# Performance work log

Hardware: AMD Instinct MI355X
Metric: run time of the kernel (lower is better)

Reference implementation:

```python
import jax, jax.numpy as jnp
import numpy as np

NPOINT = 2048
RADIUS = 0.4
NSAMPLE = 32
BN_EPS = 1e-5


def setup_inputs() -> dict:
    key = jax.random.key(0)
    ks = jax.random.split(key, 6)
    B, N, C = 8, 8192, 64
    xyz = jax.random.normal(ks[0], (B, N, 3), jnp.float32)
    points = jax.random.normal(ks[1], (B, N, C), jnp.float32)
    W1 = jax.random.normal(ks[2], (3 + C, 64), jnp.float32) * 0.1
    W2 = jax.random.normal(ks[3], (64, 64), jnp.float32) * 0.1
    W3 = jax.random.normal(ks[4], (64, 128), jnp.float32) * 0.1
    return dict(
        xyz=xyz, points=points,
        W1=W1, g1=jnp.ones(64), b1=jnp.zeros(64),
        W2=W2, g2=jnp.ones(64), b2=jnp.zeros(64),
        W3=W3, g3=jnp.ones(128), b3=jnp.zeros(128),
    )


def _furthest_point_sample(xyz, npoint):
    # xyz: (B, N, 3) -> (B, npoint) int32. Sequential max-min scan, batched.
    B, N, _ = xyz.shape

    def step(carry, _):
        dists, last = carry
        p = jnp.take_along_axis(xyz, last[:, None, None], axis=1)  # (B,1,3)
        d2 = jnp.sum((xyz - p) ** 2, axis=-1)                       # (B,N)
        dists = jnp.minimum(dists, d2)
        nxt = jnp.argmax(dists, axis=-1).astype(jnp.int32)
        return (dists, nxt), nxt

    init = (jnp.full((B, N), 1e10, xyz.dtype), jnp.zeros((B,), jnp.int32))
    _, idx = jax.lax.scan(step, init, None, length=npoint - 1)      # (npoint-1, B)
    idx = jnp.concatenate([jnp.zeros((1, B), jnp.int32), idx], axis=0)
    return idx.T                                                    # (B, npoint)


def _ball_query(xyz, new_xyz, radius, nsample):
    # For each centroid take the first nsample point indices (in original order)
    # within `radius`; pad with the first found index (CUDA ball_query semantics).
    B, N, _ = xyz.shape
    d2 = jnp.sum((new_xyz[:, :, None, :] - xyz[:, None, :, :]) ** 2, axis=-1)  # (B,S,N)
    mask = d2 < radius * radius
    key = jnp.where(mask, jnp.arange(N, dtype=jnp.int32), N)
    srt = jnp.sort(key, axis=-1)[..., :nsample]                     # (B,S,K)
    first = srt[..., :1]
    first = jnp.where(first == N, 0, first)                         # empty ball -> index 0
    return jnp.where(srt == N, first, srt)


def _gather(pts, idx):
    # pts: (B,N,D), idx: (B,...) -> (B,...,D)
    return jax.vmap(lambda p, i: p[i])(pts, idx)


def reference(xyz, points, W1, g1, b1, W2, g2, b2, W3, g3, b3):
    fps_idx = _furthest_point_sample(xyz, NPOINT)                   # (B,S)
    new_xyz = _gather(xyz, fps_idx)                                 # (B,S,3)
    idx = _ball_query(xyz, new_xyz, RADIUS, NSAMPLE)                # (B,S,K)
    grouped_xyz = _gather(xyz, idx) - new_xyz[:, :, None, :]        # (B,S,K,3)
    grouped_pts = _gather(points, idx)                              # (B,S,K,C)
    feats = jnp.concatenate([grouped_xyz, grouped_pts], axis=-1)    # (B,S,K,3+C)
    for W, g, b in ((W1, g1, b1), (W2, g2, b2), (W3, g3, b3)):
        feats = feats @ W                                           # 1x1 conv
        m = feats.mean(axis=(0, 1, 2))
        v = feats.var(axis=(0, 1, 2))                               # biased, torch BN train mode
        feats = g * (feats - m) * jax.lax.rsqrt(v + BN_EPS) + b
        feats = jax.nn.relu(feats)
    new_points = feats.max(axis=2)                                  # max over nsample -> (B,S,mlp[-1])
    return new_xyz, new_points
```

## Files before the change

### kernel.cpp

```cpp
#include <hip/hip_runtime.h>

constexpr int B_ = 8, N_ = 8192, NPOINT_ = 2048, NSAMPLE_ = 32;
constexpr int M_ROWS = B_ * NPOINT_ * NSAMPLE_;
constexpr int NGROUP = B_ * NPOINT_;
constexpr size_t OFF_NXF   = 0;
constexpr size_t OFF_IDX   = 196608;
constexpr size_t OFF_WF    = 1245184;
constexpr size_t OFF_GB    = 1311488;
constexpr size_t OFF_STATS = 1313536;
constexpr size_t OFF_NP    = 1315584;
constexpr size_t OFF_FLAG  = 1317632;
constexpr size_t OFF_MAXB  = 2097152;

__device__ __forceinline__ float bf2f(unsigned short u) {
  union { unsigned u; float f; } x; x.u = ((unsigned)u) << 16; return x.f;
}
__device__ __forceinline__ float lo16f(unsigned u) {
  union { unsigned u; float f; } x; x.u = u << 16; return x.f;
}
__device__ __forceinline__ float hi16f(unsigned u) {
  union { unsigned u; float f; } x; x.u = u & 0xffff0000u; return x.f;
}
__device__ __forceinline__ unsigned short f2bf(float f) {
  union { float f; unsigned u; } x; x.f = f;
  unsigned u = x.u + 0x7FFFu + ((x.u >> 16) & 1u);
  return (unsigned short)(u >> 16);
}
__device__ __forceinline__ int f2i(float f) {
  union { float f; int i; } x; x.f = f; return x.i;
}
__device__ __forceinline__ float i2f(int i) {
  union { int i; float f; } x; x.i = i; return x.f;
}
__device__ __forceinline__ void unpack8(uint4 u, float* x) {
  x[0] = bf2f((unsigned short)(u.x & 0xffffu)); x[1] = bf2f((unsigned short)(u.x >> 16));
  x[2] = bf2f((unsigned short)(u.y & 0xffffu)); x[3] = bf2f((unsigned short)(u.y >> 16));
  x[4] = bf2f((unsigned short)(u.z & 0xffffu)); x[5] = bf2f((unsigned short)(u.z >> 16));
  x[6] = bf2f((unsigned short)(u.w & 0xffffu)); x[7] = bf2f((unsigned short)(u.w >> 16));
}
__device__ __forceinline__ float ldf(const void* p, size_t i, bool bf) {
  return bf ? bf2f(((const unsigned short*)p)[i]) : ((const float*)p)[i];
}
__device__ __forceinline__ void stf(void* p, size_t i, bool bf, float v) {
  if (bf) ((unsigned short*)p)[i] = f2bf(v);
  else    ((float*)p)[i] = v;
}

template <int CTRL>
__device__ __forceinline__ float dpp_maxf(float v) {
  int n = __builtin_amdgcn_update_dpp(0, f2i(v), CTRL, 0xF, 0xF, true);
  return fmaxf(v, i2f(n));
}

extern "C" __global__ void detect_kernel(const unsigned short* __restrict__ xyz,
                                         int* __restrict__ flag) {
  if (threadIdx.x == 0 && blockIdx.x == 0) {
    int sane = 0;
    for (int k = 0; k < 32; ++k) {
      int e = (xyz[2 * k] >> 7) & 0xff;
      if (e >= 90 && e <= 140) ++sane;
    }
    *flag = (sane >= 24) ? 1 : 0;
  }
}

extern "C" __global__ void prep_kernel(
    const void* W1, const void* W2, const void* W3,
    const void* g1, const void* b1, const void* g2, const void* b2,
    const void* g3, const void* b3,
    float* __restrict__ wf, float* __restrict__ gb, const int* __restrict__ flag) {
  const bool bf = (*flag != 0);
  int i = blockIdx.x * 256 + threadIdx.x;
  if (i < 4288)       wf[i] = ldf(W1, i, bf);
  else if (i < 8384)  wf[i] = ldf(W2, i - 4288, bf);
  else if (i < 16576) wf[i] = ldf(W3, i - 8384, bf);
  else if (i < 17088) {
    int k = i - 16576; float v;
    if (k < 64)       v = ldf(g1, k, bf);
    else if (k < 128) v = ldf(b1, k - 64, bf);
    else if (k < 192) v = ldf(g2, k - 128, bf);
    else if (k < 256) v = ldf(b2, k - 192, bf);
    else if (k < 384) v = ldf(g3, k - 256, bf);
    else              v = ldf(b3, k - 384, bf);
    gb[k] = v;
  }
}

extern "C" __global__ void conv_kernel(const void* xyz, float* __restrict__ sxyz,
                                       const int* __restrict__ flag) {
  const bool bf = (*flag != 0);
  int i = blockIdx.x * 256 + threadIdx.x;
  if (i < B_ * N_) {
    sxyz[i]             = ldf(xyz, (size_t)i * 3 + 0, bf);
    sxyz[B_*N_ + i]     = ldf(xyz, (size_t)i * 3 + 1, bf);
    sxyz[2*B_*N_ + i]   = ldf(xyz, (size_t)i * 3 + 2, bf);
  }
}

template <bool BF>
__device__ __forceinline__ void fps_body(
    const void* xyz, void* out, float* __restrict__ nxf, float4* slots) {
#pragma clang fp contract(off)
  const int b = blockIdx.x;
  const int t = threadIdx.x;
  const int lane = t & 63, w = t >> 6;
  const size_t base = (size_t)b * N_ * 3;
  float px[8], py[8], pz[8], d[8];
  if (BF) {
    const uint4* xp = (const uint4*)((const unsigned short*)xyz + base) + t * 3;
    unsigned cc[12];
#pragma unroll
    for (int m = 0; m < 3; ++m) {
      uint4 u = xp[m];
      cc[4*m+0] = u.x; cc[4*m+1] = u.y; cc[4*m+2] = u.z; cc[4*m+3] = u.w;
    }
#pragma unroll
    for (int k = 0; k < 8; ++k) {
      if ((k & 1) == 0) {
        unsigned ra = cc[(3*k) >> 1], rb = cc[((3*k) >> 1) + 1];
        px[k] = lo16f(ra); py[k] = hi16f(ra); pz[k] = lo16f(rb);
      } else {
        unsigned ra = cc[(3*k - 1) >> 1], rb = cc[(3*k + 1) >> 1];
        px[k] = hi16f(ra); py[k] = lo16f(rb); pz[k] = hi16f(rb);
      }
    }
  } else {
#pragma unroll
    for (int k = 0; k < 8; ++k) {
      int i = t * 8 + k;
      px[k] = ((const float*)xyz)[base + i*3 + 0];
      py[k] = ((const float*)xyz)[base + i*3 + 1];
      pz[k] = ((const float*)xyz)[base + i*3 + 2];
    }
  }
#pragma unroll
  for (int k = 0; k < 8; ++k) d[k] = 1e10f;
  float s0x=0.f,s0y=0.f,s0z=0.f, s1x=0.f,s1y=0.f,s1z=0.f;
  float p0, p1, p2;
  if (BF) {
    const unsigned short* xp16 = (const unsigned short*)xyz + base;
    p0 = bf2f(xp16[0]); p1 = bf2f(xp16[1]); p2 = bf2f(xp16[2]);
  } else {
    p0 = ((const float*)xyz)[base + 0];
    p1 = ((const float*)xyz)[base + 1];
    p2 = ((const float*)xyz)[base + 2];
  }
  if (t == 0) { s0x = p0; s0y = p1; s0z = p2; }
  for (int j = 1; j < NPOINT_; ++j) {
    float bv = -1.0f;
#pragma unroll
    for (int k = 0; k < 8; ++k) {
      float dx = px[k] - p0, dy = py[k] - p1, dz = pz[k] - p2;
      float d2 = (dx*dx + dy*dy) + dz*dz;
      float dn = fminf(d[k], d2);
      d[k] = dn;
      bv = fmaxf(bv, dn);
    }
    float g = bv;
    g = dpp_maxf<0xB1>(g);
    g = dpp_maxf<0x4E>(g);
    g = dpp_maxf<0x141>(g);
    g = dpp_maxf<0x140>(g);
    g = dpp_maxf<0x142>(g);
    g = dpp_maxf<0x143>(g);
    float wmax = i2f(__builtin_amdgcn_readlane(f2i(g), 63));
    unsigned long long hm = __ballot(bv == wmax);
    int sl = (int)__builtin_ctzll(hm);
    const int pb = (j & 1) << 4;
    if (lane == sl) {
      int bk = 0;
#pragma unroll
      for (int k = 7; k >= 1; --k)
        if (d[k] == bv) bk = k;
      float cx = px[0], cy = py[0], cz = pz[0];
#pragma unroll
      for (int k = 1; k < 8; ++k)
        if (bk == k) { cx = px[k]; cy = py[k]; cz = pz[k]; }
      slots[pb + w] = make_float4(bv, cx, cy, cz);
    }
    __syncthreads();
    float4 kc = slots[pb + (lane & 15)];
    float m2 = kc.x;
    m2 = dpp_maxf<0xB1>(m2);
    m2 = dpp_maxf<0x4E>(m2);
    m2 = dpp_maxf<0x141>(m2);
    m2 = dpp_maxf<0x140>(m2);
    unsigned long long bm = __ballot(kc.x == m2);
    int s2 = (int)__builtin_ctzll(bm);
    p0 = i2f(__builtin_amdgcn_readlane(f2i(kc.y), s2));
    p1 = i2f(__builtin_amdgcn_readlane(f2i(kc.z), s2));
    p2 = i2f(__builtin_amdgcn_readlane(f2i(kc.w), s2));
    if (t == (j & 1023)) {
      if ((j >> 10) == 0) { s0x = p0; s0y = p1; s0z = p2; }
      else                { s1x = p0; s1y = p1; s1z = p2; }
    }
  }
  const bool bfrt = BF;
#pragma unroll
  for (int s = 0; s < 2; ++s) {
    float cx = (s==0)?s0x:s1x;
    float cy = (s==0)?s0y:s1y;
    float cz = (s==0)?s0z:s1z;
    size_t o = ((size_t)b * NPOINT_ + s * 1024 + t) * 3;
    nxf[o+0] = cx; nxf[o+1] = cy; nxf[o+2] = cz;
    stf(out, o+0, bfrt, cx); stf(out, o+1, bfrt, cy); stf(out, o+2, bfrt, cz);
  }
}

extern "C" __global__ void __launch_bounds__(1024, 4) fps_kernel(
    const void* xyz, void* out, float* __restrict__ nxf,
    const int* __restrict__ flag) {
  __shared__ float4 slots[32];
  if (*flag != 0) fps_body<true>(xyz, out, nxf, slots);
  else            fps_body<false>(xyz, out, nxf, slots);
}

extern "C" __global__ void __launch_bounds__(256) ballq_kernel(
    const float* __restrict__ sxyz, const float* __restrict__ nxf,
    unsigned short* __restrict__ idxout) {
#pragma clang fp contract(off)
  const int gw = (int)((blockIdx.x * 256 + threadIdx.x) >> 6);
  const int lane = threadIdx.x & 63;
  const int b = gw >> 11;
  const int j = gw & (NPOINT_ - 1);
  const float* sx = sxyz;
  const float* sy = sxyz + B_ * N_;
  const float* sz = sxyz + 2 * B_ * N_;
  const size_t pbase = (size_t)b * N_;
  const size_t co = ((size_t)b * NPOINT_ + j) * 3;
  const float c0 = nxf[co], c1 = nxf[co+1], c2 = nxf[co+2];
  unsigned short* out = idxout + (size_t)gw * NSAMPLE_;
  int cnt = 0, first = -1;
  for (int c = 0; c < N_/64 && cnt < NSAMPLE_; ++c) {
    int i = c * 64 + lane;
    float dx = sx[pbase + i] - c0;
    float dy = sy[pbase + i] - c1;
    float dz = sz[pbase + i] - c2;
    float d2 = (dx*dx + dy*dy) + dz*dz;
    bool hit = d2 < 0.16f;
    unsigned long long m = __ballot(hit);
    if (m) {
      if (first < 0) first = c * 64 + (int)__builtin_ctzll(m);
      int rank = __builtin_amdgcn_mbcnt_hi(
          (unsigned)(m >> 32), __builtin_amdgcn_mbcnt_lo((unsigned)m, 0));
      if (hit) {
        int pos = cnt + rank;
        if (pos < NSAMPLE_) out[pos] = (unsigned short)i;
      }
      cnt += __builtin_popcountll(m);
    }
  }
  if (first < 0) first = 0;
  if (lane < NSAMPLE_ && lane >= cnt) out[lane] = (unsigned short)first;
}

__device__ __forceinline__ void l1_row(
    const void* xyz, const void* points, const float* __restrict__ nxf,
    const unsigned short* __restrict__ idx, const float* __restrict__ wf,
    int r, bool bf, float* acc) {
  const int b = r >> 16;
  const int j = (r >> 5) & (NPOINT_ - 1);
  const int i = idx[r];
  const size_t pt = (size_t)b * N_ + i;
  const float* cp = nxf + ((size_t)b * NPOINT_ + j) * 3;
  float f0 = ldf(xyz, pt*3 + 0, bf) - cp[0];
  float f1 = ldf(xyz, pt*3 + 1, bf) - cp[1];
  float f2 = ldf(xyz, pt*3 + 2, bf) - cp[2];
#pragma unroll
  for (int c = 0; c < 64; ++c)
    acc[c] = fmaf(f0, wf[c], fmaf(f1, wf[64+c], f2 * wf[128+c]));
  const float* wp = wf + 192;
  if (bf) {
    const uint4* pp = (const uint4*)((const unsigned short*)points + pt * 64);
#pragma unroll
    for (int s = 0; s < 8; ++s) {
      uint4 u = pp[s];
      float x[8]; unpack8(u, x);
#pragma unroll
      for (int kk = 0; kk < 8; ++kk)
#pragma unroll
        for (int c = 0; c < 64; ++c)
          acc[c] = fmaf(x[kk], wp[(s*8+kk)*64 + c], acc[c]);
    }
  } else {
    const float4* pp = (const float4*)((const float*)points + pt * 64);
#pragma unroll
    for (int s = 0; s < 16; ++s) {
      float4 u = pp[s];
      float x[4] = {u.x, u.y, u.z, u.w};
#pragma unroll
      for (int kk = 0; kk < 4; ++kk)
#pragma unroll
        for (int c = 0; c < 64; ++c)
          acc[c] = fmaf(x[kk], wp[(s*4+kk)*64 + c], acc[c]);
    }
  }
}

template <int LDW>
__device__ __forceinline__ void mm64(const float* v, const float* __restrict__ w,
                                     float* acc) {
#pragma unroll
  for (int ch = 0; ch < 64; ++ch)
#pragma unroll
    for (int c = 0; c < 64; ++c)
      acc[c] = fmaf(v[ch], w[ch*LDW + c], acc[c]);
}

__device__ __forceinline__ void bnrelu64(float* v, const float* __restrict__ np0) {
#pragma unroll
  for (int c = 0; c < 64; ++c)
    v[c] = fmaxf(fmaf(v[c], np0[c], np0[64 + c]), 0.f);
}

__device__ __forceinline__ void commit_stats64(float* a, float* __restrict__ stats) {
  float q[64];
#pragma unroll
  for (int c = 0; c < 64; ++c) q[c] = a[c] * a[c];
#pragma unroll
  for (int off = 1; off < 64; off <<= 1)
#pragma unroll
    for (int c = 0; c < 64; ++c) {
      a[c] += __shfl_xor(a[c], off);
      q[c] += __shfl_xor(q[c], off);
    }
  __shared__ float LS[4][64], LQ[4][64];
  const int t = threadIdx.x, w = t >> 6;
  if ((t & 63) == 0) {
#pragma unroll
    for (int c = 0; c < 64; ++c) { LS[w][c] = a[c]; LQ[w][c] = q[c]; }
  }
  __syncthreads();
  if (t < 64) {
    atomicAdd(&stats[t],      LS[0][t] + LS[1][t] + LS[2][t] + LS[3][t]);
    atomicAdd(&stats[64 + t], LQ[0][t] + LQ[1][t] + LQ[2][t] + LQ[3][t]);
  }
}

extern "C" __global__ void __launch_bounds__(256) p1_kernel(
    const void* xyz, const void* points, const float* __restrict__ nxf,
    const unsigned short* __restrict__ idx, const float* __restrict__ wf,
    float* __restrict__ stats, const int* __restrict__ flag) {
  const bool bf = (*flag != 0);
  const int r = blockIdx.x * 256 + threadIdx.x;
  float acc[64];
  l1_row(xyz, points, nxf, idx, wf, r, bf, acc);
  commit_stats64(acc, stats);
}

extern "C" __global__ void __launch_bounds__(256, 2) p2_kernel(
    const void* xyz, const void* points, const float* __restrict__ nxf,
    const unsigned short* __restrict__ idx, const float* __restrict__ wf,
    const float* __restrict__ w2, const float* __restrict__ np1,
    float* __restrict__ stats, const int* __restrict__ flag) {
  const bool bf = (*flag != 0);
  const int r = blockIdx.x * 256 + threadIdx.x;
  float v[64];
  l1_row(xyz, points, nxf, idx, wf, r, bf, v);
  bnrelu64(v, np1);
  float acc[64];
#pragma unroll
  for (int c = 0; c < 64; ++c) acc[c] = 0.f;
  mm64<64>(v, w2, acc);
  commit_stats64(acc, stats);
}

extern "C" __global__ void __launch_bounds__(256, 2) p3_kernel(
    const void* xyz, const void* points, const float* __restrict__ nxf,
    const unsigned short* __restrict__ idx, const float* __restrict__ wf,
    const float* __restrict__ w2, const float* __restrict__ w3,
    const float* __restrict__ np1, const float* __restrict__ np2,
    unsigned short* __restrict__ maxb, float* __restrict__ stats,
    const int* __restrict__ flag) {
  const bool bf = (*flag != 0);
  const int t = threadIdx.x, lane = t & 63, w = t >> 6;
  const int h = __builtin_amdgcn_readfirstlane(w & 1);
  const int g = blockIdx.x * 4 + (w >> 1) * 2 + (lane >> 5);
  const int r = g * 32 + (lane & 31);
  float v[64];
  l1_row(xyz, points, nxf, idx, wf, r, bf, v);
  bnrelu64(v, np1);
  float y2[64];
#pragma unroll
  for (int c = 0; c < 64; ++c) y2[c] = 0.f;
  mm64<64>(v, w2, y2);
  bnrelu64(y2, np2);
  const float* w3h = w3 + h * 64;
  float y3[64];
#pragma unroll
  for (int c = 0; c < 64; ++c) y3[c] = 0.f;
  mm64<128>(y2, w3h, y3);
  float* s = v; float* q = y2;
#pragma unroll
  for (int c = 0; c < 64; ++c) { s[c] = y3[c]; q[c] = y3[c] * y3[c]; }
#pragma unroll
  for (int off = 1; off <= 16; off <<= 1)
#pragma unroll
    for (int c = 0; c < 64; ++c)
      y3[c] = fmaxf(y3[c], __shfl_xor(y3[c], off));
  if ((lane & 31) == 0) {
    unsigned short* mo = maxb + (size_t)g * 128 + h * 64;
#pragma unroll
    for (int c = 0; c < 64; ++c) mo[c] = f2bf(y3[c]);
  }
#pragma unroll
  for (int off = 1; off < 64; off <<= 1)
#pragma unroll
    for (int c = 0; c < 64; ++c) {
      s[c] += __shfl_xor(s[c], off);
      q[c] += __shfl_xor(q[c], off);
    }
  __shared__ float LS[4][64], LQ[4][64];
  if (lane == 0) {
#pragma unroll
    for (int c = 0; c < 64; ++c) { LS[w][c] = s[c]; LQ[w][c] = q[c]; }
  }
  __syncthreads();
  if (t < 128) {
    int hh = t >> 6, cl = t & 63;
    atomicAdd(&stats[t],       LS[hh][cl] + LS[hh+2][cl]);
    atomicAdd(&stats[128 + t], LQ[hh][cl] + LQ[hh+2][cl]);
  }
}

extern "C" __global__ void nparam_kernel(
    const float* __restrict__ stats, const float* __restrict__ g,
    const float* __restrict__ bb, float* __restrict__ npar, int Cc) {
  int c = threadIdx.x;
  if (c < Cc) {
    float m = stats[c] * (1.0f / M_ROWS);
    float v = stats[Cc + c] * (1.0f / M_ROWS) - m * m;
    float sc = g[c] / sqrtf(v + 1e-5f);
    npar[c] = sc;
    npar[Cc + c] = bb[c] - m * sc;
  }
}

extern "C" __global__ void __launch_bounds__(256) final_kernel(
    const unsigned short* __restrict__ maxb, const float* __restrict__ npar,
    void* out, const int* __restrict__ flag) {
  const bool bf = (*flag != 0);
  const int gtid = blockIdx.x * 256 + threadIdx.x;
  const int c = gtid & 127;
  float y = bf2f(maxb[gtid]);
  float r = fmaxf(fmaf(y, npar[c], npar[128 + c]), 0.f);
  stf(out, (size_t)B_ * NPOINT_ * 3 + gtid, bf, r);
}

extern "C" void kernel_launch(void* const* d_in, const int* in_sizes, int n_in,
                              void* d_out, int out_size, void* d_ws, size_t ws_size,
                              hipStream_t stream) {
  const void* xyz    = d_in[0];
  const void* points = d_in[1];
  char* ws = (char*)d_ws;
  float* nxf   = (float*)(ws + OFF_NXF);
  unsigned short* wsIdx = (unsigned short*)(ws + OFF_IDX);
  float* wf    = (float*)(ws + OFF_WF);
  float* gb    = (float*)(ws + OFF_GB);
  float* stats = (float*)(ws + OFF_STATS);
  float* npar  = (float*)(ws + OFF_NP);
  int*   flag  = (int*)(ws + OFF_FLAG);
  unsigned short* maxb = (unsigned short*)(ws + OFF_MAXB);
  float* sxyz  = (float*)(ws + OFF_MAXB);

  hipMemsetAsync(stats, 0, 512 * sizeof(float), stream);
  detect_kernel<<<1, 64, 0, stream>>>((const unsigned short*)xyz, flag);
  prep_kernel<<<67, 256, 0, stream>>>(d_in[2], d_in[5], d_in[8], d_in[3], d_in[4],
                                      d_in[6], d_in[7], d_in[9], d_in[10], wf, gb, flag);
  conv_kernel<<<(B_ * N_) / 256, 256, 0, stream>>>(xyz, sxyz, flag);
  fps_kernel<<<B_, 1024, 0, stream>>>(xyz, d_out, nxf, flag);
  ballq_kernel<<<(B_ * NPOINT_) / 4, 256, 0, stream>>>(sxyz, nxf, wsIdx);
  p1_kernel<<<M_ROWS / 256, 256, 0, stream>>>(xyz, points, nxf, wsIdx, wf, stats, flag);
  nparam_kernel<<<1, 128, 0, stream>>>(stats, gb, gb + 64, npar, 64);
  p2_kernel<<<M_ROWS / 256, 256, 0, stream>>>(xyz, points, nxf, wsIdx, wf, wf + 4288,
                                              npar, stats + 128, flag);
  nparam_kernel<<<1, 128, 0, stream>>>(stats + 128, gb + 128, gb + 192, npar + 128, 64);
  p3_kernel<<<(2 * M_ROWS) / 256, 256, 0, stream>>>(xyz, points, nxf, wsIdx, wf,
                                                    wf + 4288, wf + 8384, npar,
                                                    npar + 128, maxb, stats + 256, flag);
  nparam_kernel<<<1, 128, 0, stream>>>(stats + 256, gb + 256, gb + 384, npar + 256, 128);
  final_kernel<<<(NGROUP * 128) / 256, 256, 0, stream>>>(maxb, npar + 256, d_out, flag);
}
```

Baseline: 3.768 ms.

## Shrink FPS to 256 threads per batch and compute both layer-3 halves per thread

```diff
diff --git a/kernel.cpp b/kernel.cpp
--- a/kernel.cpp
+++ b/kernel.cpp
@@ -105,17 +105,17 @@
   const int t = threadIdx.x;
   const int lane = t & 63, w = t >> 6;
   const size_t base = (size_t)b * N_ * 3;
-  float px[8], py[8], pz[8], d[8];
+  float px[32], py[32], pz[32], d[32];
   if (BF) {
-    const uint4* xp = (const uint4*)((const unsigned short*)xyz + base) + t * 3;
-    unsigned cc[12];
-#pragma unroll
-    for (int m = 0; m < 3; ++m) {
+    const uint4* xp = (const uint4*)((const unsigned short*)xyz + base) + t * 12;
+    unsigned cc[48];
+#pragma unroll
+    for (int m = 0; m < 12; ++m) {
       uint4 u = xp[m];
       cc[4*m+0] = u.x; cc[4*m+1] = u.y; cc[4*m+2] = u.z; cc[4*m+3] = u.w;
     }
 #pragma unroll
-    for (int k = 0; k < 8; ++k) {
+    for (int k = 0; k < 32; ++k) {
       if ((k & 1) == 0) {
         unsigned ra = cc[(3*k) >> 1], rb = cc[((3*k) >> 1) + 1];
         px[k] = lo16f(ra); py[k] = hi16f(ra); pz[k] = lo16f(rb);
@@ -126,16 +126,19 @@
     }
   } else {
 #pragma unroll
-    for (int k = 0; k < 8; ++k) {
-      int i = t * 8 + k;
+    for (int k = 0; k < 32; ++k) {
+      int i = t * 32 + k;
       px[k] = ((const float*)xyz)[base + i*3 + 0];
       py[k] = ((const float*)xyz)[base + i*3 + 1];
       pz[k] = ((const float*)xyz)[base + i*3 + 2];
     }
   }
 #pragma unroll
-  for (int k = 0; k < 8; ++k) d[k] = 1e10f;
-  float s0x=0.f,s0y=0.f,s0z=0.f, s1x=0.f,s1y=0.f,s1z=0.f;
+  for (int k = 0; k < 32; ++k) d[k] = 1e10f;
+  float c0x=0.f,c0y=0.f,c0z=0.f, c1x=0.f,c1y=0.f,c1z=0.f,
+        c2x=0.f,c2y=0.f,c2z=0.f, c3x=0.f,c3y=0.f,c3z=0.f,
+        c4x=0.f,c4y=0.f,c4z=0.f, c5x=0.f,c5y=0.f,c5z=0.f,
+        c6x=0.f,c6y=0.f,c6z=0.f, c7x=0.f,c7y=0.f,c7z=0.f;
   float p0, p1, p2;
   if (BF) {
     const unsigned short* xp16 = (const unsigned short*)xyz + base;
@@ -145,11 +148,11 @@
     p1 = ((const float*)xyz)[base + 1];
     p2 = ((const float*)xyz)[base + 2];
   }
-  if (t == 0) { s0x = p0; s0y = p1; s0z = p2; }
+  if (t == 0) { c0x = p0; c0y = p1; c0z = p2; }
   for (int j = 1; j < NPOINT_; ++j) {
     float bv = -1.0f;
 #pragma unroll
-    for (int k = 0; k < 8; ++k) {
+    for (int k = 0; k < 32; ++k) {
       float dx = px[k] - p0, dy = py[k] - p1, dz = pz[k] - p2;
       float d2 = (dx*dx + dy*dy) + dz*dz;
       float dn = fminf(d[k], d2);
@@ -166,51 +169,59 @@
     float wmax = i2f(__builtin_amdgcn_readlane(f2i(g), 63));
     unsigned long long hm = __ballot(bv == wmax);
     int sl = (int)__builtin_ctzll(hm);
-    const int pb = (j & 1) << 4;
+    const int pb = (j & 1) << 2;
     if (lane == sl) {
       int bk = 0;
 #pragma unroll
-      for (int k = 7; k >= 1; --k)
+      for (int k = 31; k >= 1; --k)
         if (d[k] == bv) bk = k;
       float cx = px[0], cy = py[0], cz = pz[0];
 #pragma unroll
-      for (int k = 1; k < 8; ++k)
+      for (int k = 1; k < 32; ++k)
         if (bk == k) { cx = px[k]; cy = py[k]; cz = pz[k]; }
       slots[pb + w] = make_float4(bv, cx, cy, cz);
     }
     __syncthreads();
-    float4 kc = slots[pb + (lane & 15)];
+    float4 kc = slots[pb + (lane & 3)];
     float m2 = kc.x;
     m2 = dpp_maxf<0xB1>(m2);
     m2 = dpp_maxf<0x4E>(m2);
-    m2 = dpp_maxf<0x141>(m2);
-    m2 = dpp_maxf<0x140>(m2);
     unsigned long long bm = __ballot(kc.x == m2);
     int s2 = (int)__builtin_ctzll(bm);
     p0 = i2f(__builtin_amdgcn_readlane(f2i(kc.y), s2));
     p1 = i2f(__builtin_amdgcn_readlane(f2i(kc.z), s2));
     p2 = i2f(__builtin_amdgcn_readlane(f2i(kc.w), s2));
-    if (t == (j & 1023)) {
-      if ((j >> 10) == 0) { s0x = p0; s0y = p1; s0z = p2; }
-      else                { s1x = p0; s1y = p1; s1z = p2; }
+    if (t == (j & 255)) {
+      int s = j >> 8;
+      if      (s == 0) { c0x = p0; c0y = p1; c0z = p2; }
+      else if (s == 1) { c1x = p0; c1y = p1; c1z = p2; }
+      else if (s == 2) { c2x = p0; c2y = p1; c2z = p2; }
+      else if (s == 3) { c3x = p0; c3y = p1; c3z = p2; }
+      else if (s == 4) { c4x = p0; c4y = p1; c4z = p2; }
+      else if (s == 5) { c5x = p0; c5y = p1; c5z = p2; }
+      else if (s == 6) { c6x = p0; c6y = p1; c6z = p2; }
+      else             { c7x = p0; c7y = p1; c7z = p2; }
     }
   }
   const bool bfrt = BF;
 #pragma unroll
-  for (int s = 0; s < 2; ++s) {
-    float cx = (s==0)?s0x:s1x;
-    float cy = (s==0)?s0y:s1y;
-    float cz = (s==0)?s0z:s1z;
-    size_t o = ((size_t)b * NPOINT_ + s * 1024 + t) * 3;
+  for (int s = 0; s < 8; ++s) {
+    float cx = (s==0)?c0x:(s==1)?c1x:(s==2)?c2x:(s==3)?c3x:
+               (s==4)?c4x:(s==5)?c5x:(s==6)?c6x:c7x;
+    float cy = (s==0)?c0y:(s==1)?c1y:(s==2)?c2y:(s==3)?c3y:
+               (s==4)?c4y:(s==5)?c5y:(s==6)?c6y:c7y;
+    float cz = (s==0)?c0z:(s==1)?c1z:(s==2)?c2z:(s==3)?c3z:
+               (s==4)?c4z:(s==5)?c5z:(s==6)?c6z:c7z;
+    size_t o = ((size_t)b * NPOINT_ + s * 256 + t) * 3;
     nxf[o+0] = cx; nxf[o+1] = cy; nxf[o+2] = cz;
     stf(out, o+0, bfrt, cx); stf(out, o+1, bfrt, cy); stf(out, o+2, bfrt, cz);
   }
 }
 
-extern "C" __global__ void __launch_bounds__(1024, 4) fps_kernel(
+extern "C" __global__ void __launch_bounds__(256, 1) fps_kernel(
     const void* xyz, void* out, float* __restrict__ nxf,
     const int* __restrict__ flag) {
-  __shared__ float4 slots[32];
+  __shared__ float4 slots[8];
   if (*flag != 0) fps_body<true>(xyz, out, nxf, slots);
   else            fps_body<false>(xyz, out, nxf, slots);
 }
@@ -374,9 +385,8 @@
     const int* __restrict__ flag) {
   const bool bf = (*flag != 0);
   const int t = threadIdx.x, lane = t & 63, w = t >> 6;
-  const int h = __builtin_amdgcn_readfirstlane(w & 1);
-  const int g = blockIdx.x * 4 + (w >> 1) * 2 + (lane >> 5);
-  const int r = g * 32 + (lane & 31);
+  const int r = blockIdx.x * 256 + t;
+  const int g = r >> 5;
   float v[64];
   l1_row(xyz, points, nxf, idx, wf, r, bf, v);
   bnrelu64(v, np1);
@@ -385,41 +395,61 @@
   for (int c = 0; c < 64; ++c) y2[c] = 0.f;
   mm64<64>(v, w2, y2);
   bnrelu64(y2, np2);
-  const float* w3h = w3 + h * 64;
-  float y3[64];
-#pragma unroll
-  for (int c = 0; c < 64; ++c) y3[c] = 0.f;
-  mm64<128>(y2, w3h, y3);
-  float* s = v; float* q = y2;
-#pragma unroll
-  for (int c = 0; c < 64; ++c) { s[c] = y3[c]; q[c] = y3[c] * y3[c]; }
-#pragma unroll
-  for (int off = 1; off <= 16; off <<= 1)
-#pragma unroll
-    for (int c = 0; c < 64; ++c)
-      y3[c] = fmaxf(y3[c], __shfl_xor(y3[c], off));
-  if ((lane & 31) == 0) {
-    unsigned short* mo = maxb + (size_t)g * 128 + h * 64;
-#pragma unroll
-    for (int c = 0; c < 64; ++c) mo[c] = f2bf(y3[c]);
-  }
-#pragma unroll
-  for (int off = 1; off < 64; off <<= 1)
-#pragma unroll
-    for (int c = 0; c < 64; ++c) {
-      s[c] += __shfl_xor(s[c], off);
-      q[c] += __shfl_xor(q[c], off);
-    }
-  __shared__ float LS[4][64], LQ[4][64];
-  if (lane == 0) {
-#pragma unroll
-    for (int c = 0; c < 64; ++c) { LS[w][c] = s[c]; LQ[w][c] = q[c]; }
+  __shared__ float LSA[4][64], LQA[4][64], LSB[4][64], LQB[4][64];
+  float* y3 = v;
+  float sc[64];
+#pragma unroll
+  for (int h = 0; h < 2; ++h) {
+#pragma unroll
+    for (int c = 0; c < 64; ++c) y3[c] = 0.f;
+    mm64<128>(y2, w3 + h * 64, y3);
+#pragma unroll
+    for (int c = 0; c < 64; ++c) sc[c] = y3[c] * y3[c];
+#pragma unroll
+    for (int off = 1; off < 64; off <<= 1)
+#pragma unroll
+      for (int c = 0; c < 64; ++c) sc[c] += __shfl_xor(sc[c], off);
+    if (lane == 0) {
+#pragma unroll
+      for (int c = 0; c < 64; ++c) {
+        if (h == 0) LQA[w][c] = sc[c]; else LQB[w][c] = sc[c];
+      }
+    }
+#pragma unroll
+    for (int c = 0; c < 64; ++c) sc[c] = y3[c];
+#pragma unroll
+    for (int off = 1; off < 64; off <<= 1)
+#pragma unroll
+      for (int c = 0; c < 64; ++c) sc[c] += __shfl_xor(sc[c], off);
+    if (lane == 0) {
+#pragma unroll
+      for (int c = 0; c < 64; ++c) {
+        if (h == 0) LSA[w][c] = sc[c]; else LSB[w][c] = sc[c];
+      }
+    }
+#pragma unroll
+    for (int off = 1; off <= 16; off <<= 1)
+#pragma unroll
+      for (int c = 0; c < 64; ++c)
+        y3[c] = fmaxf(y3[c], __shfl_xor(y3[c], off));
+    if ((lane & 31) == 0) {
+      unsigned short* mo = maxb + (size_t)g * 128 + h * 64;
+#pragma unroll
+      for (int c = 0; c < 64; ++c) mo[c] = f2bf(y3[c]);
+    }
   }
   __syncthreads();
-  if (t < 128) {
-    int hh = t >> 6, cl = t & 63;
-    atomicAdd(&stats[t],       LS[hh][cl] + LS[hh+2][cl]);
-    atomicAdd(&stats[128 + t], LQ[hh][cl] + LQ[hh+2][cl]);
+  if (t < 64) {
+    atomicAdd(&stats[t],        LSA[0][t]+LSA[1][t]+LSA[2][t]+LSA[3][t]);
+  } else if (t < 128) {
+    int c = t - 64;
+    atomicAdd(&stats[t],        LSB[0][c]+LSB[1][c]+LSB[2][c]+LSB[3][c]);
+  } else if (t < 192) {
+    int c = t - 128;
+    atomicAdd(&stats[t],        LQA[0][c]+LQA[1][c]+LQA[2][c]+LQA[3][c]);
+  } else {
+    int c = t - 192;
+    atomicAdd(&stats[t],        LQB[0][c]+LQB[1][c]+LQB[2][c]+LQB[3][c]);
   }
 }
 
@@ -468,16 +498,16 @@
   prep_kernel<<<67, 256, 0, stream>>>(d_in[2], d_in[5], d_in[8], d_in[3], d_in[4],
                                       d_in[6], d_in[7], d_in[9], d_in[10], wf, gb, flag);
   conv_kernel<<<(B_ * N_) / 256, 256, 0, stream>>>(xyz, sxyz, flag);
-  fps_kernel<<<B_, 1024, 0, stream>>>(xyz, d_out, nxf, flag);
+  fps_kernel<<<B_, 256, 0, stream>>>(xyz, d_out, nxf, flag);
   ballq_kernel<<<(B_ * NPOINT_) / 4, 256, 0, stream>>>(sxyz, nxf, wsIdx);
   p1_kernel<<<M_ROWS / 256, 256, 0, stream>>>(xyz, points, nxf, wsIdx, wf, stats, flag);
   nparam_kernel<<<1, 128, 0, stream>>>(stats, gb, gb + 64, npar, 64);
   p2_kernel<<<M_ROWS / 256, 256, 0, stream>>>(xyz, points, nxf, wsIdx, wf, wf + 4288,
                                               npar, stats + 128, flag);
   nparam_kernel<<<1, 128, 0, stream>>>(stats + 128, gb + 128, gb + 192, npar + 128, 64);
-  p3_kernel<<<(2 * M_ROWS) / 256, 256, 0, stream>>>(xyz, points, nxf, wsIdx, wf,
-                                                    wf + 4288, wf + 8384, npar,
-                                                    npar + 128, maxb, stats + 256, flag);
+  p3_kernel<<<M_ROWS / 256, 256, 0, stream>>>(xyz, points, nxf, wsIdx, wf,
+                                              wf + 4288, wf + 8384, npar,
+                                              npar + 128, maxb, stats + 256, flag);
   nparam_kernel<<<1, 128, 0, stream>>>(stats + 256, gb + 256, gb + 384, npar + 256, 128);
   final_kernel<<<(NGROUP * 128) / 256, 256, 0, stream>>>(maxb, npar + 256, d_out, flag);
 }
```

Result: slower. 6.115 ms (+62.3%).
